# Optimization experiments

Hardware: AMD Instinct MI355X
Metric: run time of the kernel (lower is better)

The kernel has to match this reference:

```python
import jax, jax.numpy as jnp
import numpy as np

N, C, K, H = 100000, 128, 16, 128
MIX_IN = 2 * C + 1 + C   # x, mean_feat, boundary_score, coord_embed
GATE_IN = 2 * C + 1


def _mlp2(x, w1, b1, w2, b2):
    # Linear -> GELU(exact) -> Linear (dropout=0 at eval)
    return jax.nn.gelu(x @ w1 + b1, approximate=False) @ w2 + b2


def setup_inputs() -> dict:
    key = jax.random.key(0)
    ks = jax.random.split(key, 16)
    s = 0.02
    return {
        "feats": jax.random.normal(ks[0], (N, C), jnp.float32),
        "points": jax.random.normal(ks[1], (N, 3), jnp.float32),
        "neighbors": jax.random.randint(ks[2], (N, K), 0, N, jnp.int64),
        "ln_g": jnp.ones((C,), jnp.float32),
        "ln_b": jnp.zeros((C,), jnp.float32),
        "cp_w1": jax.random.normal(ks[3], (3, H), jnp.float32) * s,
        "cp_b1": jnp.zeros((H,), jnp.float32),
        "cp_w2": jax.random.normal(ks[4], (H, C), jnp.float32) * s,
        "cp_b2": jnp.zeros((C,), jnp.float32),
        "bd_w1": jax.random.normal(ks[5], (2, H), jnp.float32) * s,
        "bd_b1": jnp.zeros((H,), jnp.float32),
        "bd_w2": jax.random.normal(ks[6], (H, 1), jnp.float32) * s,
        "bd_b2": jnp.zeros((1,), jnp.float32),
        "mix_w1": jax.random.normal(ks[7], (MIX_IN, H), jnp.float32) * s,
        "mix_b1": jnp.zeros((H,), jnp.float32),
        "mix_w2": jax.random.normal(ks[8], (H, C), jnp.float32) * s,
        "mix_b2": jnp.zeros((C,), jnp.float32),
        "gate_w1": jax.random.normal(ks[9], (GATE_IN, H), jnp.float32) * s,
        "gate_b1": jnp.zeros((H,), jnp.float32),
        "gate_w2": jax.random.normal(ks[10], (H, C), jnp.float32) * s,
        "gate_b2": jnp.zeros((C,), jnp.float32),
        "out_w": jax.random.normal(ks[11], (C, C), jnp.float32) * s,
        "out_b": jnp.zeros((C,), jnp.float32),
    }


def _forward(feats, points, neighbors, ln_g, ln_b, cp_w1, cp_b1, cp_w2, cp_b2,
             bd_w1, bd_b1, bd_w2, bd_b2, mix_w1, mix_b1, mix_w2, mix_b2,
             gate_w1, gate_b1, gate_w2, gate_b2, out_w, out_b):
    n = feats.shape[0]
    # LayerNorm (eps=1e-5, torch default)
    mu = feats.mean(-1, keepdims=True)
    var = jnp.mean((feats - mu) ** 2, -1, keepdims=True)
    x = (feats - mu) * jax.lax.rsqrt(var + 1e-5) * ln_g + ln_b

    # sanitize neighbors
    valid = ((neighbors >= 0) & (neighbors < n)).astype(x.dtype)  # [N,K]
    safe = jnp.clip(neighbors, 0, n - 1)

    neigh_feats = x[safe]        # [N,K,C]
    neigh_points = points[safe]  # [N,K,3]
    denom = jnp.maximum(valid.sum(1, keepdims=True), 1.0)  # [N,1]
    w = valid[..., None]
    mean_feat = (neigh_feats * w).sum(1) / denom    # [N,C]
    mean_point = (neigh_points * w).sum(1) / denom  # [N,3]

    feat_diff = jnp.linalg.norm(x - mean_feat, axis=-1, keepdims=True)       # [N,1]
    coord_diff = jnp.linalg.norm(points - mean_point, axis=-1, keepdims=True)

    boundary = jax.nn.sigmoid(_mlp2(jnp.concatenate([feat_diff, coord_diff], -1),
                                    bd_w1, bd_b1, bd_w2, bd_b2))  # [N,1]

    # normalize points globally
    centered = points - points.mean(0, keepdims=True)
    scale = jnp.maximum(jnp.abs(centered).max(0, keepdims=True), 1e-6)
    coord_embed = _mlp2(centered / scale, cp_w1, cp_b1, cp_w2, cp_b2)  # [N,C]

    refined = _mlp2(jnp.concatenate([x, mean_feat, boundary, coord_embed], -1),
                    mix_w1, mix_b1, mix_w2, mix_b2)
    gate = jax.nn.sigmoid(_mlp2(jnp.concatenate([x, mean_feat, boundary], -1),
                                gate_w1, gate_b1, gate_w2, gate_b2))
    refined = (gate * refined) @ out_w + out_b
    return feats + refined


def reference(feats, points, neighbors, ln_g, ln_b, cp_w1, cp_b1, cp_w2, cp_b2,
              bd_w1, bd_b1, bd_w2, bd_b2, mix_w1, mix_b1, mix_w2, mix_b2,
              gate_w1, gate_b1, gate_w2, gate_b2, out_w, out_b):
    return _forward(feats, points, neighbors, ln_g, ln_b, cp_w1, cp_b1, cp_w2, cp_b2,
                    bd_w1, bd_b1, bd_w2, bd_b2, mix_w1, mix_b1, mix_w2, mix_b2,
                    gate_w1, gate_b1, gate_w2, gate_b2, out_w, out_b)
```

## Files before the change

kernel.cpp:

```cpp
#include <hip/hip_runtime.h>
#include <math.h>

constexpr int C    = 128;
constexpr int K    = 16;
constexpr int H    = 128;
constexpr int NB2  = 256;
constexpr int WPTS = 32;
constexpr int PB   = 128;
constexpr int HSU  = 68;

constexpr int WT_MIX   = 0;
constexpr int WT_GATE  = 49152;
constexpr int WT_CP2   = 81920;
constexpr int WT_MIX2  = 98304;
constexpr int WT_GATE2 = 114688;
constexpr int WT_OUT   = 131072;
constexpr int WT_TOTAL = 147456;

typedef __attribute__((ext_vector_type(8))) short short8;
typedef __attribute__((ext_vector_type(4))) float f32x4;
typedef _Float16 h2 __attribute__((ext_vector_type(2)));

__device__ __forceinline__ short f2bf(float f) {
    unsigned u = __float_as_uint(f);
    unsigned r = (u + 0x7fffu + ((u >> 16) & 1u)) >> 16;
    return (short)r;
}
__device__ __forceinline__ unsigned cvt_pk_bf16(float lo, float hi) {
    unsigned r;
    asm("v_cvt_pk_bf16_f32 %0, %1, %2" : "=v"(r) : "v"(lo), "v"(hi));
    return r;
}
__device__ __forceinline__ float bflo(unsigned v) { return __uint_as_float(v << 16); }
__device__ __forceinline__ float bfhi(unsigned v) { return __uint_as_float(v & 0xffff0000u); }
__device__ __forceinline__ float rcpf(float v) { return __builtin_amdgcn_rcpf(v); }

__device__ __forceinline__ unsigned f2e5m2(float x) {
    union { _Float16 h; unsigned short u; } cv;
    cv.h = (_Float16)x;
    return ((unsigned)cv.u + 0x7Fu + ((cv.u >> 8) & 1u)) >> 8;
}

__device__ __forceinline__ float gelu_f(float x) {
    float a = fabsf(x) * 0.70710678118654752440f;
    float t = rcpf(1.0f + 0.3275911f * a);
    float p = t * (0.254829592f + t * (-0.284496736f + t * (1.421413741f
            + t * (-1.453152027f + t * 1.061405429f))));
    float e = __expf(-a * a);
    float er = 1.0f - p * e;
    return 0.5f * x * (1.0f + copysignf(er, x));
}
__device__ __forceinline__ float sigm(float v) { return rcpf(1.0f + __expf(-v)); }

__global__ __launch_bounds__(256) void prep_all(
    const float* __restrict__ mix_w1, const float* __restrict__ gate_w1,
    const float* __restrict__ cp_w2,  const float* __restrict__ mix_w2,
    const float* __restrict__ gate_w2, const float* __restrict__ out_w,
    const float* __restrict__ points, const float* __restrict__ feats,
    const float* __restrict__ ln_g, const float* __restrict__ ln_b,
    short* __restrict__ wt, unsigned* __restrict__ xb,
    unsigned short* __restrict__ xg, float* __restrict__ pts4,
    float* __restrict__ partial, int n, int np4)
{
    __shared__ float sm[256];
    const int b   = blockIdx.x;
    const int tid = threadIdx.x;

    if (b < 36) {
        const float* src; int off; int c; bool skip256 = false;
        if (b < 12)      { src = mix_w1;  off = WT_MIX;   c = b;      skip256 = true; }
        else if (b < 20) { src = gate_w1; off = WT_GATE;  c = b - 12; }
        else if (b < 24) { src = cp_w2;   off = WT_CP2;   c = b - 20; }
        else if (b < 28) { src = mix_w2;  off = WT_MIX2;  c = b - 24; }
        else if (b < 32) { src = gate_w2; off = WT_GATE2; c = b - 28; }
        else             { src = out_w;   off = WT_OUT;   c = b - 32; }
        for (int ii = 0; ii < 16; ++ii) {
            int e = ii * 256 + tid;
            int j = e & 7, l = (e >> 3) & 63, t = e >> 9;
            int k = c * 32 + ((l >> 4) * 8) + j;
            int nn = t * 16 + (l & 15);
            int kk = (skip256 && k >= 256) ? k + 1 : k;
            wt[off + c * 4096 + e] = f2bf(src[kk * C + nn]);
        }
        return;
    }
    if (b == 36) {
        if (tid < 64) xb[(size_t)n * 64 + tid] = 0u;
        else if (tid < 96) ((unsigned*)xg)[(size_t)n * 32 + (tid - 64)] = 0u;
        return;
    }
    if (b < 37 + np4) {
        int i = (b - 37) * 256 + tid;
        if (i < n) {
            pts4[i * 4 + 0] = points[i * 3 + 0];
            pts4[i * 4 + 1] = points[i * 3 + 1];
            pts4[i * 4 + 2] = points[i * 3 + 2];
            pts4[i * 4 + 3] = 0.0f;
        } else if (i == n) {
            pts4[i * 4 + 0] = 0.0f; pts4[i * 4 + 1] = 0.0f;
            pts4[i * 4 + 2] = 0.0f; pts4[i * 4 + 3] = 0.0f;
        }
        return;
    }
    if (b < 37 + np4 + NB2) {
        const int bb = b - 37 - np4;
        float s[3] = {0, 0, 0};
        float mn[3] = {1e30f, 1e30f, 1e30f};
        float mx[3] = {-1e30f, -1e30f, -1e30f};
        for (int i = bb * 256 + tid; i < n; i += NB2 * 256) {
            #pragma unroll
            for (int c = 0; c < 3; ++c) {
                float v = points[i * 3 + c];
                s[c] += v; mn[c] = fminf(mn[c], v); mx[c] = fmaxf(mx[c], v);
            }
        }
        for (int q = 0; q < 9; ++q) {
            float v = (q < 3) ? s[q] : (q < 6) ? mn[q - 3] : mx[q - 6];
            sm[tid] = v;
            __syncthreads();
            for (int o = 128; o > 0; o >>= 1) {
                if (tid < o) {
                    float a = sm[tid], c = sm[tid + o];
                    sm[tid] = (q < 3) ? a + c : (q < 6) ? fminf(a, c) : fmaxf(a, c);
                }
                __syncthreads();
            }
            if (tid == 0) partial[bb * 9 + q] = sm[0];
            __syncthreads();
        }
        return;
    }

    const int lane = tid & 63;
    const int wave = tid >> 6;
    const int i = (b - 37 - np4 - NB2) * 4 + wave;
    if (i >= n) return;
    const float2 f = *(const float2*)(feats + i * C + 2 * lane);
    float s = f.x + f.y;
    #pragma unroll
    for (int o = 32; o > 0; o >>= 1) s += __shfl_xor(s, o, 64);
    const float mu = s * (1.0f / C);
    const float d0 = f.x - mu, d1 = f.y - mu;
    float v = d0 * d0 + d1 * d1;
    #pragma unroll
    for (int o = 32; o > 0; o >>= 1) v += __shfl_xor(v, o, 64);
    const float rs = rsqrtf(v * (1.0f / C) + 1e-5f);
    const float x0 = d0 * rs * ln_g[2 * lane] + ln_b[2 * lane];
    const float x1 = d1 * rs * ln_g[2 * lane + 1] + ln_b[2 * lane + 1];
    xb[(size_t)i * 64 + lane] =
        (unsigned)(unsigned short)f2bf(x0) | ((unsigned)(unsigned short)f2bf(x1) << 16);
    xg[(size_t)i * 64 + lane] =
        (unsigned short)(f2e5m2(x0) | (f2e5m2(x1) << 8));
}

__global__ __launch_bounds__(256, 2) void main_kernel(
    const unsigned* __restrict__ xb, const unsigned* __restrict__ xg,
    const float* __restrict__ pts4, const float* __restrict__ feats,
    const int* __restrict__ neighbors,
    const float* __restrict__ partial, const short* __restrict__ wt,
    const float* __restrict__ cp_w1, const float* __restrict__ cp_b1,
    const float* __restrict__ cp_b2,
    const float* __restrict__ bd_w1, const float* __restrict__ bd_b1,
    const float* __restrict__ bd_w2, const float* __restrict__ bd_b2,
    const float* __restrict__ mix_w1, const float* __restrict__ mix_b1,
    const float* __restrict__ mix_b2,
    const float* __restrict__ gate_w1, const float* __restrict__ gate_b1,
    const float* __restrict__ gate_b2,
    const float* __restrict__ out_b,
    float* __restrict__ out, int n)
{
    __shared__ __align__(16) char lds[71168];
    unsigned* mf_s  = (unsigned*)lds;
    unsigned* hid_s = (unsigned*)(lds + 34816);
    float* denom_s  = (float*)(lds + 69632);
    float* cd_s     = denom_s + 128;
    float* bd_s     = cd_s + 128;

    const int tid  = threadIdx.x;
    const int lane = tid & 63;
    const int w    = tid >> 6;
    const int m16  = lane & 15;
    const int h4   = lane >> 4;
    const int i0   = blockIdx.x * PB;
    const int wv32 = w * WPTS;
    const int i0w  = i0 + wv32;
    int* nb_w = (int*)(hid_s + (size_t)wv32 * HSU);

    {
        const int p0 = lane >> 2;
        const int jb = 4 * (lane & 3);
        const int r0 = min(i0w + p0, n - 1);
        const int r1 = min(i0w + 16 + p0, n - 1);
        const int4 A0 = *(const int4*)(neighbors + (size_t)r0 * K + jb);
        const int4 A1 = *(const int4*)(neighbors + (size_t)r1 * K + jb);

        const int q00 = ((unsigned)A0.x < (unsigned)n) ? A0.x : n;
        const int q01 = ((unsigned)A0.y < (unsigned)n) ? A0.y : n;
        const int q02 = ((unsigned)A0.z < (unsigned)n) ? A0.z : n;
        const int q03 = ((unsigned)A0.w < (unsigned)n) ? A0.w : n;
        const int q10 = ((unsigned)A1.x < (unsigned)n) ? A1.x : n;
        const int q11 = ((unsigned)A1.y < (unsigned)n) ? A1.y : n;
        const int q12 = ((unsigned)A1.z < (unsigned)n) ? A1.z : n;
        const int q13 = ((unsigned)A1.w < (unsigned)n) ? A1.w : n;

        *(int4*)&nb_w[4 * lane]       = make_int4(q00, q01, q02, q03);
        *(int4*)&nb_w[256 + 4 * lane] = make_int4(q10, q11, q12, q13);

        float c0 = (float)((q00 != n) + (q01 != n) + (q02 != n) + (q03 != n));
        float c1 = (float)((q10 != n) + (q11 != n) + (q12 != n) + (q13 != n));
        c0 += __shfl_xor(c0, 1, 64); c0 += __shfl_xor(c0, 2, 64);
        c1 += __shfl_xor(c1, 1, 64); c1 += __shfl_xor(c1, 2, 64);
        const float d0 = fmaxf(c0, 1.0f), d1 = fmaxf(c1, 1.0f);
        if ((lane & 3) == 0) {
            denom_s[wv32 + p0]      = d0;
            denom_s[wv32 + 16 + p0] = d1;
        }

        f32x4 s0 = *(const f32x4*)(pts4 + 4 * q00);
        s0 += *(const f32x4*)(pts4 + 4 * q01);
        s0 += *(const f32x4*)(pts4 + 4 * q02);
        s0 += *(const f32x4*)(pts4 + 4 * q03);
        f32x4 s1 = *(const f32x4*)(pts4 + 4 * q10);
        s1 += *(const f32x4*)(pts4 + 4 * q11);
        s1 += *(const f32x4*)(pts4 + 4 * q12);
        s1 += *(const f32x4*)(pts4 + 4 * q13);
        #pragma unroll
        for (int c = 0; c < 3; ++c) {
            s0[c] += __shfl_xor(s0[c], 1, 64); s0[c] += __shfl_xor(s0[c], 2, 64);
            s1[c] += __shfl_xor(s1[c], 1, 64); s1[c] += __shfl_xor(s1[c], 2, 64);
        }
        if ((lane & 3) == 0) {
            const float rd0 = rcpf(d0), rd1 = rcpf(d1);
            const f32x4 pv0 = *(const f32x4*)(pts4 + 4 * r0);
            const f32x4 pv1 = *(const f32x4*)(pts4 + 4 * r1);
            const float e00 = pv0[0] - s0[0] * rd0, e01 = pv0[1] - s0[1] * rd0, e02 = pv0[2] - s0[2] * rd0;
            const float e10 = pv1[0] - s1[0] * rd1, e11 = pv1[1] - s1[1] * rd1, e12 = pv1[2] - s1[2] * rd1;
            cd_s[wv32 + p0]      = sqrtf(e00 * e00 + e01 * e01 + e02 * e02);
            cd_s[wv32 + 16 + p0] = sqrtf(e10 * e10 + e11 * e11 + e12 * e12);
        }
    }

    float mean0, mean1, mean2, rsc0, rsc1, rsc2;
    {
        float sx = 0, sy = 0, sz = 0;
        float mnx = 1e30f, mny = 1e30f, mnz = 1e30f;
        float mxx = -1e30f, mxy = -1e30f, mxz = -1e30f;
        #pragma unroll
        for (int t = 0; t < 4; ++t) {
            const float* pp = partial + (size_t)(lane + 64 * t) * 9;
            sx += pp[0]; sy += pp[1]; sz += pp[2];
            mnx = fminf(mnx, pp[3]); mny = fminf(mny, pp[4]); mnz = fminf(mnz, pp[5]);
            mxx = fmaxf(mxx, pp[6]); mxy = fmaxf(mxy, pp[7]); mxz = fmaxf(mxz, pp[8]);
        }
        #pragma unroll
        for (int o = 32; o > 0; o >>= 1) {
            sx += __shfl_xor(sx, o, 64); sy += __shfl_xor(sy, o, 64); sz += __shfl_xor(sz, o, 64);
            mnx = fminf(mnx, __shfl_xor(mnx, o, 64));
            mny = fminf(mny, __shfl_xor(mny, o, 64));
            mnz = fminf(mnz, __shfl_xor(mnz, o, 64));
            mxx = fmaxf(mxx, __shfl_xor(mxx, o, 64));
            mxy = fmaxf(mxy, __shfl_xor(mxy, o, 64));
            mxz = fmaxf(mxz, __shfl_xor(mxz, o, 64));
        }
        const float fn = (float)n;
        mean0 = sx / fn; mean1 = sy / fn; mean2 = sz / fn;
        rsc0 = rcpf(fmaxf(fmaxf(mxx - mean0, mean0 - mnx), 1e-6f));
        rsc1 = rcpf(fmaxf(fmaxf(mxy - mean1, mean1 - mny), 1e-6f));
        rsc2 = rcpf(fmaxf(fmaxf(mxz - mean2, mean2 - mnz), 1e-6f));
    }

    {
        const int ul   = lane & 31;
        const int half = lane >> 5;
        float w1f[4], w1c[4], b1v[4], w2v[4];
        #pragma unroll
        for (int j = 0; j < 4; ++j) {
            int u = ul + 32 * j;
            w1f[j] = bd_w1[u]; w1c[j] = bd_w1[H + u];
            b1v[j] = bd_b1[u]; w2v[j] = bd_w2[u];
        }
        const float bb2 = bd_b2[0];

        unsigned B0[16], B1[16], B2[16], B3[16];

        auto bstep = [&](unsigned (&cur)[16], unsigned (&pf)[16], int pr, bool do_pf) {
            if (do_pf) {
                #pragma unroll
                for (int k = 0; k < K; ++k)
                    pf[k] = xg[(size_t)nb_w[((pr + 2) * 2 + half) * K + k] * 32 + ul];
            }
            union UH { unsigned u; h2 h; };
            UH a02, a13; a02.u = 0u; a13.u = 0u;
            #pragma unroll
            for (int k = 0; k < K; ++k) {
                const unsigned u = cur[k];
                UH lo, hi;
                lo.u = (u << 8) & 0xFF00FF00u;
                hi.u = u & 0xFF00FF00u;
                a02.h += lo.h;
                a13.h += hi.h;
            }
            float f0 = (float)a02.h[0], f2 = (float)a02.h[1];
            float f1 = (float)a13.h[0], f3 = (float)a13.h[1];

            const int p = 2 * pr + half;
            const float rden = rcpf(denom_s[wv32 + p]);
            f0 *= rden; f1 *= rden; f2 *= rden; f3 *= rden;
            uint2 pk;
            pk.x = cvt_pk_bf16(f0, f1);
            pk.y = cvt_pk_bf16(f2, f3);
            *(uint2*)(mf_s + (size_t)(wv32 + p) * HSU + 2 * ul) = pk;

            const int ipp = min(i0w + p, n - 1);
            const uint2 xv = *(const uint2*)(xb + (size_t)ipp * 64 + 2 * ul);
            const float d0 = bflo(xv.x) - f0, d1 = bfhi(xv.x) - f1;
            const float d2 = bflo(xv.y) - f2, d3 = bfhi(xv.y) - f3;
            float ss = d0 * d0 + d1 * d1 + d2 * d2 + d3 * d3;
            #pragma unroll
            for (int o = 16; o > 0; o >>= 1) ss += __shfl_xor(ss, o, 64);
            const float fd = sqrtf(ss);
            const float cd = cd_s[wv32 + p];
            float s = 0.0f;
            #pragma unroll
            for (int j = 0; j < 4; ++j)
                s += gelu_f(fd * w1f[j] + cd * w1c[j] + b1v[j]) * w2v[j];
            #pragma unroll
            for (int o = 16; o > 0; o >>= 1) s += __shfl_xor(s, o, 64);
            if (ul == 0) bd_s[wv32 + p] = sigm(s + bb2);
        };

        #pragma unroll
        for (int k = 0; k < K; ++k)
            B0[k] = xg[(size_t)nb_w[(0 + half) * K + k] * 32 + ul];
        #pragma unroll
        for (int k = 0; k < K; ++k)
            B1[k] = xg[(size_t)nb_w[(2 + half) * K + k] * 32 + ul];

        for (int g = 0; g < 3; ++g) {
            const int pr = 4 * g;
            bstep(B0, B2, pr + 0, true);
            bstep(B1, B3, pr + 1, true);
            bstep(B2, B0, pr + 2, true);
            bstep(B3, B1, pr + 3, true);
        }
        bstep(B0, B2, 12, true);
        bstep(B1, B3, 13, true);
        bstep(B2, B0, 14, false);
        bstep(B3, B1, 15, false);
    }

    const int pr0 = wv32 + m16, pr1 = wv32 + 16 + m16;
    const int ig0 = i0 + pr0,   ig1 = i0 + pr1;
    const int ip0 = min(ig0, n - 1), ip1 = min(ig1, n - 1);
    const unsigned* xr0  = xb + (size_t)ip0 * 64;
    const unsigned* xr1  = xb + (size_t)ip1 * 64;
    const unsigned* mfr0 = mf_s + pr0 * HSU;
    const unsigned* mfr1 = mf_s + pr1 * HSU;
    unsigned* hr0 = hid_s + pr0 * HSU;
    unsigned* hr1 = hid_s + pr1 * HSU;

    const float bdp0 = bd_s[pr0], bdp1 = bd_s[pr1];

    {
        f32x4 a0[8], a1[8];
        #pragma unroll
        for (int t = 0; t < 8; ++t) { a0[t] = (f32x4)0.0f; a1[t] = (f32x4)0.0f; }
        __builtin_amdgcn_s_setprio(1);
        #pragma unroll
        for (int c = 0; c < 8; ++c) {
            short8 af0, af1;
            if (c < 4) {
                af0 = *(const short8*)(xr0 + c * 16 + h4 * 4);
                af1 = *(const short8*)(xr1 + c * 16 + h4 * 4);
            } else {
                af0 = *(const short8*)(mfr0 + (c - 4) * 16 + h4 * 4);
                af1 = *(const short8*)(mfr1 + (c - 4) * 16 + h4 * 4);
            }
            const short* wgc = wt + WT_GATE + c * 4096 + lane * 8;
            #pragma unroll
            for (int t = 0; t < 8; ++t) {
                const short8 wf = *(const short8*)(wgc + t * 512);
                a0[t] = __builtin_amdgcn_mfma_f32_16x16x32_bf16(wf, af0, a0[t], 0, 0, 0);
                a1[t] = __builtin_amdgcn_mfma_f32_16x16x32_bf16(wf, af1, a1[t], 0, 0, 0);
            }
        }
        __builtin_amdgcn_s_setprio(0);
        #pragma unroll
        for (int t = 0; t < 8; ++t) {
            const int col = t * 16 + h4 * 4;
            const f32x4 wb = *(const f32x4*)(gate_w1 + 256 * C + col);
            const f32x4 bb = *(const f32x4*)(gate_b1 + col);
            const f32x4 v0 = a0[t] + bdp0 * wb + bb;
            const f32x4 v1 = a1[t] + bdp1 * wb + bb;
            uint2 pk0, pk1;
            pk0.x = cvt_pk_bf16(gelu_f(v0[0]), gelu_f(v0[1]));
            pk0.y = cvt_pk_bf16(gelu_f(v0[2]), gelu_f(v0[3]));
            pk1.x = cvt_pk_bf16(gelu_f(v1[0]), gelu_f(v1[1]));
            pk1.y = cvt_pk_bf16(gelu_f(v1[2]), gelu_f(v1[3]));
            *(uint2*)(hr0 + 8 * t + 2 * h4) = pk0;
            *(uint2*)(hr1 + 8 * t + 2 * h4) = pk1;
        }
    }

    uint2 gpk0[8], gpk1[8];
    {
        f32x4 a0[8], a1[8];
        #pragma unroll
        for (int t = 0; t < 8; ++t) { a0[t] = (f32x4)0.0f; a1[t] = (f32x4)0.0f; }
        __builtin_amdgcn_s_setprio(1);
        #pragma unroll
        for (int c = 0; c < 4; ++c) {
            const short8 af0 = *(const short8*)(hr0 + c * 16 + h4 * 4);
            const short8 af1 = *(const short8*)(hr1 + c * 16 + h4 * 4);
            const short* wgc = wt + WT_GATE2 + c * 4096 + lane * 8;
            #pragma unroll
            for (int t = 0; t < 8; ++t) {
                const short8 wf = *(const short8*)(wgc + t * 512);
                a0[t] = __builtin_amdgcn_mfma_f32_16x16x32_bf16(wf, af0, a0[t], 0, 0, 0);
                a1[t] = __builtin_amdgcn_mfma_f32_16x16x32_bf16(wf, af1, a1[t], 0, 0, 0);
            }
        }
        __builtin_amdgcn_s_setprio(0);
        #pragma unroll
        for (int t = 0; t < 8; ++t) {
            const f32x4 bb = *(const f32x4*)(gate_b2 + t * 16 + h4 * 4);
            gpk0[t].x = cvt_pk_bf16(sigm(a0[t][0] + bb[0]), sigm(a0[t][1] + bb[1]));
            gpk0[t].y = cvt_pk_bf16(sigm(a0[t][2] + bb[2]), sigm(a0[t][3] + bb[3]));
            gpk1[t].x = cvt_pk_bf16(sigm(a1[t][0] + bb[0]), sigm(a1[t][1] + bb[1]));
            gpk1[t].y = cvt_pk_bf16(sigm(a1[t][2] + bb[2]), sigm(a1[t][3] + bb[3]));
        }
    }

    {
        const f32x4 pv0 = *(const f32x4*)(pts4 + 4 * ip0);
        const f32x4 pv1 = *(const f32x4*)(pts4 + 4 * ip1);
        const float px0 = (pv0[0] - mean0) * rsc0;
        const float py0 = (pv0[1] - mean1) * rsc1;
        const float pz0 = (pv0[2] - mean2) * rsc2;
        const float px1 = (pv1[0] - mean0) * rsc0;
        const float py1 = (pv1[1] - mean1) * rsc1;
        const float pz1 = (pv1[2] - mean2) * rsc2;
        f32x4 a0[8], a1[8];
        #pragma unroll
        for (int t = 0; t < 8; ++t) { a0[t] = (f32x4)0.0f; a1[t] = (f32x4)0.0f; }
        #pragma unroll
        for (int c = 0; c < 4; ++c) {
            union { unsigned u[4]; short8 s; } cu0, cu1;
            #pragma unroll
            for (int jj = 0; jj < 4; ++jj) {
                const int hh = c * 32 + h4 * 8 + 2 * jj;
                const float wa0 = cp_w1[hh],     wb0 = cp_w1[H + hh],     wc0 = cp_w1[2 * H + hh];
                const float wa1 = cp_w1[hh + 1], wb1 = cp_w1[H + hh + 1], wc1 = cp_w1[2 * H + hh + 1];
                const float bb0 = cp_b1[hh], bb1 = cp_b1[hh + 1];
                cu0.u[jj] = cvt_pk_bf16(gelu_f(bb0 + px0 * wa0 + py0 * wb0 + pz0 * wc0),
                                        gelu_f(bb1 + px0 * wa1 + py0 * wb1 + pz0 * wc1));
                cu1.u[jj] = cvt_pk_bf16(gelu_f(bb0 + px1 * wa0 + py1 * wb0 + pz1 * wc0),
                                        gelu_f(bb1 + px1 * wa1 + py1 * wb1 + pz1 * wc1));
            }
            const short* wcp = wt + WT_CP2 + c * 4096 + lane * 8;
            __builtin_amdgcn_s_setprio(1);
            #pragma unroll
            for (int t = 0; t < 8; ++t) {
                const short8 wf = *(const short8*)(wcp + t * 512);
                a0[t] = __builtin_amdgcn_mfma_f32_16x16x32_bf16(wf, cu0.s, a0[t], 0, 0, 0);
                a1[t] = __builtin_amdgcn_mfma_f32_16x16x32_bf16(wf, cu1.s, a1[t], 0, 0, 0);
            }
            __builtin_amdgcn_s_setprio(0);
        }
        #pragma unroll
        for (int t = 0; t < 8; ++t) {
            const f32x4 bb = *(const f32x4*)(cp_b2 + t * 16 + h4 * 4);
            const f32x4 v0 = a0[t] + bb, v1 = a1[t] + bb;
            uint2 pk0, pk1;
            pk0.x = cvt_pk_bf16(v0[0], v0[1]); pk0.y = cvt_pk_bf16(v0[2], v0[3]);
            pk1.x = cvt_pk_bf16(v1[0], v1[1]); pk1.y = cvt_pk_bf16(v1[2], v1[3]);
            *(uint2*)(hr0 + 8 * t + 2 * h4) = pk0;
            *(uint2*)(hr1 + 8 * t + 2 * h4) = pk1;
        }
    }

    {
        f32x4 a0[8], a1[8];
        #pragma unroll
        for (int t = 0; t < 8; ++t) { a0[t] = (f32x4)0.0f; a1[t] = (f32x4)0.0f; }
        __builtin_amdgcn_s_setprio(1);
        #pragma unroll
        for (int c = 0; c < 12; ++c) {
            short8 af0, af1;
            if (c < 4) {
                af0 = *(const short8*)(xr0 + c * 16 + h4 * 4);
                af1 = *(const short8*)(xr1 + c * 16 + h4 * 4);
            } else if (c < 8) {
                af0 = *(const short8*)(mfr0 + (c - 4) * 16 + h4 * 4);
                af1 = *(const short8*)(mfr1 + (c - 4) * 16 + h4 * 4);
            } else {
                af0 = *(const short8*)(hr0 + (c - 8) * 16 + h4 * 4);
                af1 = *(const short8*)(hr1 + (c - 8) * 16 + h4 * 4);
            }
            const short* wmc = wt + WT_MIX + c * 4096 + lane * 8;
            #pragma unroll
            for (int t = 0; t < 8; ++t) {
                const short8 wf = *(const short8*)(wmc + t * 512);
                a0[t] = __builtin_amdgcn_mfma_f32_16x16x32_bf16(wf, af0, a0[t], 0, 0, 0);
                a1[t] = __builtin_amdgcn_mfma_f32_16x16x32_bf16(wf, af1, a1[t], 0, 0, 0);
            }
        }
        __builtin_amdgcn_s_setprio(0);
        #pragma unroll
        for (int t = 0; t < 8; ++t) {
            const int col = t * 16 + h4 * 4;
            const f32x4 wb = *(const f32x4*)(mix_w1 + 256 * C + col);
            const f32x4 bb = *(const f32x4*)(mix_b1 + col);
            const f32x4 v0 = a0[t] + bdp0 * wb + bb;
            const f32x4 v1 = a1[t] + bdp1 * wb + bb;
            uint2 pk0, pk1;
            pk0.x = cvt_pk_bf16(gelu_f(v0[0]), gelu_f(v0[1]));
            pk0.y = cvt_pk_bf16(gelu_f(v0[2]), gelu_f(v0[3]));
            pk1.x = cvt_pk_bf16(gelu_f(v1[0]), gelu_f(v1[1]));
            pk1.y = cvt_pk_bf16(gelu_f(v1[2]), gelu_f(v1[3]));
            *(uint2*)(hr0 + 8 * t + 2 * h4) = pk0;
            *(uint2*)(hr1 + 8 * t + 2 * h4) = pk1;
        }
    }

    {
        f32x4 a0[8], a1[8];
        #pragma unroll
        for (int t = 0; t < 8; ++t) { a0[t] = (f32x4)0.0f; a1[t] = (f32x4)0.0f; }
        __builtin_amdgcn_s_setprio(1);
        #pragma unroll
        for (int c = 0; c < 4; ++c) {
            const short8 af0 = *(const short8*)(hr0 + c * 16 + h4 * 4);
            const short8 af1 = *(const short8*)(hr1 + c * 16 + h4 * 4);
            const short* wmc = wt + WT_MIX2 + c * 4096 + lane * 8;
            #pragma unroll
            for (int t = 0; t < 8; ++t) {
                const short8 wf = *(const short8*)(wmc + t * 512);
                a0[t] = __builtin_amdgcn_mfma_f32_16x16x32_bf16(wf, af0, a0[t], 0, 0, 0);
                a1[t] = __builtin_amdgcn_mfma_f32_16x16x32_bf16(wf, af1, a1[t], 0, 0, 0);
            }
        }
        __builtin_amdgcn_s_setprio(0);
        #pragma unroll
        for (int t = 0; t < 8; ++t) {
            const f32x4 bb = *(const f32x4*)(mix_b2 + t * 16 + h4 * 4);
            const f32x4 v0 = a0[t] + bb, v1 = a1[t] + bb;
            uint2 pk0, pk1;
            pk0.x = cvt_pk_bf16(bflo(gpk0[t].x) * v0[0], bfhi(gpk0[t].x) * v0[1]);
            pk0.y = cvt_pk_bf16(bflo(gpk0[t].y) * v0[2], bfhi(gpk0[t].y) * v0[3]);
            pk1.x = cvt_pk_bf16(bflo(gpk1[t].x) * v1[0], bfhi(gpk1[t].x) * v1[1]);
            pk1.y = cvt_pk_bf16(bflo(gpk1[t].y) * v1[2], bfhi(gpk1[t].y) * v1[3]);
            *(uint2*)(hr0 + 8 * t + 2 * h4) = pk0;
            *(uint2*)(hr1 + 8 * t + 2 * h4) = pk1;
        }
    }

    {
        f32x4 a0[8], a1[8];
        #pragma unroll
        for (int t = 0; t < 8; ++t) { a0[t] = (f32x4)0.0f; a1[t] = (f32x4)0.0f; }
        __builtin_amdgcn_s_setprio(1);
        #pragma unroll
        for (int c = 0; c < 4; ++c) {
            const short8 af0 = *(const short8*)(hr0 + c * 16 + h4 * 4);
            const short8 af1 = *(const short8*)(hr1 + c * 16 + h4 * 4);
            const short* woc = wt + WT_OUT + c * 4096 + lane * 8;
            #pragma unroll
            for (int t = 0; t < 8; ++t) {
                const short8 wf = *(const short8*)(woc + t * 512);
                a0[t] = __builtin_amdgcn_mfma_f32_16x16x32_bf16(wf, af0, a0[t], 0, 0, 0);
                a1[t] = __builtin_amdgcn_mfma_f32_16x16x32_bf16(wf, af1, a1[t], 0, 0, 0);
            }
        }
        __builtin_amdgcn_s_setprio(0);
        #pragma unroll
        for (int t = 0; t < 8; ++t) {
            const int col = t * 16 + h4 * 4;
            const f32x4 bb = *(const f32x4*)(out_b + col);
            const f32x4 fv0 = *(const f32x4*)(feats + (size_t)ip0 * C + col);
            const f32x4 fv1 = *(const f32x4*)(feats + (size_t)ip1 * C + col);
            const f32x4 v0 = a0[t] + bb + fv0;
            const f32x4 v1 = a1[t] + bb + fv1;
            if (ig0 < n) *(f32x4*)(out + (size_t)ig0 * C + col) = v0;
            if (ig1 < n) *(f32x4*)(out + (size_t)ig1 * C + col) = v1;
        }
    }
}

extern "C" void kernel_launch(void* const* d_in, const int* in_sizes, int n_in,
                              void* d_out, int out_size, void* d_ws, size_t ws_size,
                              hipStream_t stream)
{
    const float* feats     = (const float*)d_in[0];
    const float* points    = (const float*)d_in[1];
    const int*   neighbors = (const int*)d_in[2];
    const float* ln_g      = (const float*)d_in[3];
    const float* ln_b      = (const float*)d_in[4];
    const float* cp_w1     = (const float*)d_in[5];
    const float* cp_b1     = (const float*)d_in[6];
    const float* cp_w2     = (const float*)d_in[7];
    const float* cp_b2     = (const float*)d_in[8];
    const float* bd_w1     = (const float*)d_in[9];
    const float* bd_b1     = (const float*)d_in[10];
    const float* bd_w2     = (const float*)d_in[11];
    const float* bd_b2     = (const float*)d_in[12];
    const float* mix_w1    = (const float*)d_in[13];
    const float* mix_b1    = (const float*)d_in[14];
    const float* mix_w2    = (const float*)d_in[15];
    const float* mix_b2    = (const float*)d_in[16];
    const float* gate_w1   = (const float*)d_in[17];
    const float* gate_b1   = (const float*)d_in[18];
    const float* gate_w2   = (const float*)d_in[19];
    const float* gate_b2   = (const float*)d_in[20];
    const float* out_w     = (const float*)d_in[21];
    const float* out_b     = (const float*)d_in[22];
    float* out = (float*)d_out;
    (void)n_in; (void)out_size; (void)ws_size;

    const int n = in_sizes[0] / C;

    char* base = (char*)d_ws;
    unsigned* xb        = (unsigned*)base;
    unsigned short* xg  = (unsigned short*)(base + (size_t)(n + 1) * 256);
    float* pts4         = (float*)(base + (size_t)(n + 1) * 384);
    short* wt           = (short*)((char*)pts4 + (size_t)(n + 1) * 16);
    float* partial      = (float*)((char*)wt + (size_t)WT_TOTAL * 2);

    const int np4 = (n + 256) / 256;
    const int nln = (n + 3) / 4;
    const int nb_main = (n + PB - 1) / PB;

    prep_all<<<37 + np4 + NB2 + nln, 256, 0, stream>>>(
        mix_w1, gate_w1, cp_w2, mix_w2, gate_w2, out_w,
        points, feats, ln_g, ln_b,
        wt, xb, xg, pts4, partial, n, np4);
    main_kernel<<<nb_main, 256, 0, stream>>>(
        xb, (const unsigned*)xg, pts4, feats, neighbors, partial, wt,
        cp_w1, cp_b1, cp_b2, bd_w1, bd_b1, bd_w2, bd_b2,
        mix_w1, mix_b1, mix_b2, gate_w1, gate_b1, gate_b2,
        out_b, out, n);
}
```

Measured before the change: 309.2 us.

## Process each wave's 32 points in two 16-point passes to double occupancy

Each wave now handles its 32 points as two sequential passes of 16 rows instead of running two 16-row MFMA tiles in parallel. This halves the accumulator registers and shrinks the LDS staging buffers (mf_s stride reduced, neighbor lists split into two buffers), so launch bounds can be raised from 2 to 4 blocks per CU. The intent is more waves in flight to hide the random neighbor gathers. The cost is that each weight fragment loaded from global memory now feeds one MFMA instead of two, doubling weight traffic per point.

```diff
diff --git a/kernel.cpp b/kernel.cpp
--- a/kernel.cpp
+++ b/kernel.cpp
@@ -8,6 +8,7 @@
 constexpr int WPTS = 32;
 constexpr int PB   = 128;
 constexpr int HSU  = 68;
+constexpr int MFU  = 66;
 
 constexpr int WT_MIX   = 0;
 constexpr int WT_GATE  = 49152;
@@ -153,7 +154,7 @@
         (unsigned short)(f2e5m2(x0) | (f2e5m2(x1) << 8));
 }
 
-__global__ __launch_bounds__(256, 2) void main_kernel(
+__global__ __launch_bounds__(256, 4) void main_kernel(
     const unsigned* __restrict__ xb, const unsigned* __restrict__ xg,
     const float* __restrict__ pts4, const float* __restrict__ feats,
     const int* __restrict__ neighbors,
@@ -169,12 +170,13 @@
     const float* __restrict__ out_b,
     float* __restrict__ out, int n)
 {
-    __shared__ __align__(16) char lds[71168];
+    __shared__ __align__(16) char lds[39936];
     unsigned* mf_s  = (unsigned*)lds;
-    unsigned* hid_s = (unsigned*)(lds + 34816);
-    float* denom_s  = (float*)(lds + 69632);
-    float* cd_s     = denom_s + 128;
-    float* bd_s     = cd_s + 128;
+    unsigned* hid_s = (unsigned*)(lds + 16896);
+    int*      nb1_s = (int*)(lds + 34304);
+    float* denom_s  = (float*)(lds + 38400);
+    float* cd_s     = (float*)(lds + 38912);
+    float* bd_s     = (float*)(lds + 39424);
 
     const int tid  = threadIdx.x;
     const int lane = tid & 63;
@@ -184,7 +186,8 @@
     const int i0   = blockIdx.x * PB;
     const int wv32 = w * WPTS;
     const int i0w  = i0 + wv32;
-    int* nb_w = (int*)(hid_s + (size_t)wv32 * HSU);
+    int* nb0_w = (int*)(hid_s + (size_t)w * 16 * HSU);
+    int* nb1_w = nb1_s + w * 256;
 
     {
         const int p0 = lane >> 2;
@@ -203,8 +206,8 @@
         const int q12 = ((unsigned)A1.z < (unsigned)n) ? A1.z : n;
         const int q13 = ((unsigned)A1.w < (unsigned)n) ? A1.w : n;
 
-        *(int4*)&nb_w[4 * lane]       = make_int4(q00, q01, q02, q03);
-        *(int4*)&nb_w[256 + 4 * lane] = make_int4(q10, q11, q12, q13);
+        *(int4*)&nb0_w[4 * lane] = make_int4(q00, q01, q02, q03);
+        *(int4*)&nb1_w[4 * lane] = make_int4(q10, q11, q12, q13);
 
         float c0 = (float)((q00 != n) + (q01 != n) + (q02 != n) + (q03 != n));
         float c1 = (float)((q10 != n) + (q11 != n) + (q12 != n) + (q13 != n));
@@ -269,320 +272,276 @@
         rsc2 = rcpf(fmaxf(fmaxf(mxz - mean2, mean2 - mnz), 1e-6f));
     }
 
-    {
-        const int ul   = lane & 31;
-        const int half = lane >> 5;
-        float w1f[4], w1c[4], b1v[4], w2v[4];
-        #pragma unroll
-        for (int j = 0; j < 4; ++j) {
-            int u = ul + 32 * j;
-            w1f[j] = bd_w1[u]; w1c[j] = bd_w1[H + u];
-            b1v[j] = bd_b1[u]; w2v[j] = bd_w2[u];
-        }
-        const float bb2 = bd_b2[0];
-
-        unsigned B0[16], B1[16], B2[16], B3[16];
-
-        auto bstep = [&](unsigned (&cur)[16], unsigned (&pf)[16], int pr, bool do_pf) {
-            if (do_pf) {
-                #pragma unroll
-                for (int k = 0; k < K; ++k)
-                    pf[k] = xg[(size_t)nb_w[((pr + 2) * 2 + half) * K + k] * 32 + ul];
-            }
-            union UH { unsigned u; h2 h; };
-            UH a02, a13; a02.u = 0u; a13.u = 0u;
-            #pragma unroll
-            for (int k = 0; k < K; ++k) {
-                const unsigned u = cur[k];
-                UH lo, hi;
-                lo.u = (u << 8) & 0xFF00FF00u;
-                hi.u = u & 0xFF00FF00u;
-                a02.h += lo.h;
-                a13.h += hi.h;
-            }
-            float f0 = (float)a02.h[0], f2 = (float)a02.h[1];
-            float f1 = (float)a13.h[0], f3 = (float)a13.h[1];
-
-            const int p = 2 * pr + half;
-            const float rden = rcpf(denom_s[wv32 + p]);
-            f0 *= rden; f1 *= rden; f2 *= rden; f3 *= rden;
-            uint2 pk;
-            pk.x = cvt_pk_bf16(f0, f1);
-            pk.y = cvt_pk_bf16(f2, f3);
-            *(uint2*)(mf_s + (size_t)(wv32 + p) * HSU + 2 * ul) = pk;
-
-            const int ipp = min(i0w + p, n - 1);
-            const uint2 xv = *(const uint2*)(xb + (size_t)ipp * 64 + 2 * ul);
-            const float d0 = bflo(xv.x) - f0, d1 = bfhi(xv.x) - f1;
-            const float d2 = bflo(xv.y) - f2, d3 = bfhi(xv.y) - f3;
-            float ss = d0 * d0 + d1 * d1 + d2 * d2 + d3 * d3;
-            #pragma unroll
-            for (int o = 16; o > 0; o >>= 1) ss += __shfl_xor(ss, o, 64);
-            const float fd = sqrtf(ss);
-            const float cd = cd_s[wv32 + p];
-            float s = 0.0f;
-            #pragma unroll
-            for (int j = 0; j < 4; ++j)
-                s += gelu_f(fd * w1f[j] + cd * w1c[j] + b1v[j]) * w2v[j];
-            #pragma unroll
-            for (int o = 16; o > 0; o >>= 1) s += __shfl_xor(s, o, 64);
-            if (ul == 0) bd_s[wv32 + p] = sigm(s + bb2);
-        };
-
-        #pragma unroll
-        for (int k = 0; k < K; ++k)
-            B0[k] = xg[(size_t)nb_w[(0 + half) * K + k] * 32 + ul];
-        #pragma unroll
-        for (int k = 0; k < K; ++k)
-            B1[k] = xg[(size_t)nb_w[(2 + half) * K + k] * 32 + ul];
-
-        for (int g = 0; g < 3; ++g) {
-            const int pr = 4 * g;
-            bstep(B0, B2, pr + 0, true);
-            bstep(B1, B3, pr + 1, true);
-            bstep(B2, B0, pr + 2, true);
-            bstep(B3, B1, pr + 3, true);
-        }
-        bstep(B0, B2, 12, true);
-        bstep(B1, B3, 13, true);
-        bstep(B2, B0, 14, false);
-        bstep(B3, B1, 15, false);
-    }
-
-    const int pr0 = wv32 + m16, pr1 = wv32 + 16 + m16;
-    const int ig0 = i0 + pr0,   ig1 = i0 + pr1;
-    const int ip0 = min(ig0, n - 1), ip1 = min(ig1, n - 1);
-    const unsigned* xr0  = xb + (size_t)ip0 * 64;
-    const unsigned* xr1  = xb + (size_t)ip1 * 64;
-    const unsigned* mfr0 = mf_s + pr0 * HSU;
-    const unsigned* mfr1 = mf_s + pr1 * HSU;
-    unsigned* hr0 = hid_s + pr0 * HSU;
-    unsigned* hr1 = hid_s + pr1 * HSU;
-
-    const float bdp0 = bd_s[pr0], bdp1 = bd_s[pr1];
-
-    {
-        f32x4 a0[8], a1[8];
-        #pragma unroll
-        for (int t = 0; t < 8; ++t) { a0[t] = (f32x4)0.0f; a1[t] = (f32x4)0.0f; }
-        __builtin_amdgcn_s_setprio(1);
-        #pragma unroll
-        for (int c = 0; c < 8; ++c) {
-            short8 af0, af1;
-            if (c < 4) {
-                af0 = *(const short8*)(xr0 + c * 16 + h4 * 4);
-                af1 = *(const short8*)(xr1 + c * 16 + h4 * 4);
-            } else {
-                af0 = *(const short8*)(mfr0 + (c - 4) * 16 + h4 * 4);
-                af1 = *(const short8*)(mfr1 + (c - 4) * 16 + h4 * 4);
-            }
-            const short* wgc = wt + WT_GATE + c * 4096 + lane * 8;
+    const int ul   = lane & 31;
+    const int half = lane >> 5;
+    float w1f[4], w1c[4], b1v[4], w2v[4];
+    #pragma unroll
+    for (int j = 0; j < 4; ++j) {
+        int u = ul + 32 * j;
+        w1f[j] = bd_w1[u]; w1c[j] = bd_w1[H + u];
+        b1v[j] = bd_b1[u]; w2v[j] = bd_w2[u];
+    }
+    const float bb2 = bd_b2[0];
+
+    #pragma unroll 1
+    for (int pass = 0; pass < 2; ++pass) {
+        const int pb    = pass * 16;
+        const int* nbp  = pass ? nb1_w : nb0_w;
+        const int ibase = i0w + pb;
+
+        {
+            unsigned B0[16], B1[16], B2[16], B3[16];
+
+            auto bstep = [&](unsigned (&cur)[16], unsigned (&pf)[16], int pr, bool do_pf) {
+                if (do_pf) {
+                    #pragma unroll
+                    for (int k = 0; k < K; ++k)
+                        pf[k] = xg[(size_t)nbp[((pr + 2) * 2 + half) * K + k] * 32 + ul];
+                }
+                union UH { unsigned u; h2 h; };
+                UH a02, a13; a02.u = 0u; a13.u = 0u;
+                #pragma unroll
+                for (int k = 0; k < K; ++k) {
+                    const unsigned u = cur[k];
+                    UH lo, hi;
+                    lo.u = (u << 8) & 0xFF00FF00u;
+                    hi.u = u & 0xFF00FF00u;
+                    a02.h += lo.h;
+                    a13.h += hi.h;
+                }
+                float f0 = (float)a02.h[0], f2 = (float)a02.h[1];
+                float f1 = (float)a13.h[0], f3 = (float)a13.h[1];
+
+                const int p = 2 * pr + half;
+                const float rden = rcpf(denom_s[wv32 + pb + p]);
+                f0 *= rden; f1 *= rden; f2 *= rden; f3 *= rden;
+                uint2 pk;
+                pk.x = cvt_pk_bf16(f0, f1);
+                pk.y = cvt_pk_bf16(f2, f3);
+                *(uint2*)(mf_s + (size_t)(w * 16 + p) * MFU + 2 * ul) = pk;
+
+                const int ipp = min(ibase + p, n - 1);
+                const uint2 xv = *(const uint2*)(xb + (size_t)ipp * 64 + 2 * ul);
+                const float d0 = bflo(xv.x) - f0, d1 = bfhi(xv.x) - f1;
+                const float d2 = bflo(xv.y) - f2, d3 = bfhi(xv.y) - f3;
+                float ss = d0 * d0 + d1 * d1 + d2 * d2 + d3 * d3;
+                #pragma unroll
+                for (int o = 16; o > 0; o >>= 1) ss += __shfl_xor(ss, o, 64);
+                const float fd = sqrtf(ss);
+                const float cd = cd_s[wv32 + pb + p];
+                float s = 0.0f;
+                #pragma unroll
+                for (int j = 0; j < 4; ++j)
+                    s += gelu_f(fd * w1f[j] + cd * w1c[j] + b1v[j]) * w2v[j];
+                #pragma unroll
+                for (int o = 16; o > 0; o >>= 1) s += __shfl_xor(s, o, 64);
+                if (ul == 0) bd_s[wv32 + pb + p] = sigm(s + bb2);
+            };
+
+            #pragma unroll
+            for (int k = 0; k < K; ++k)
+                B0[k] = xg[(size_t)nbp[(0 + half) * K + k] * 32 + ul];
+            #pragma unroll
+            for (int k = 0; k < K; ++k)
+                B1[k] = xg[(size_t)nbp[(2 + half) * K + k] * 32 + ul];
+
+            bstep(B0, B2, 0, true);
+            bstep(B1, B3, 1, true);
+            bstep(B2, B0, 2, true);
+            bstep(B3, B1, 3, true);
+            bstep(B0, B2, 4, true);
+            bstep(B1, B3, 5, true);
+            bstep(B2, B0, 6, false);
+            bstep(B3, B1, 7, false);
+        }
+
+        const int row = w * 16 + m16;
+        const int ig0 = i0 + wv32 + pb + m16;
+        const int ip0 = min(ig0, n - 1);
+        const unsigned* xr0  = xb + (size_t)ip0 * 64;
+        const unsigned* mfr0 = mf_s + row * MFU;
+        unsigned* hr0 = hid_s + row * HSU;
+        const float bdp0 = bd_s[wv32 + pb + m16];
+
+        {
+            f32x4 a[8];
+            #pragma unroll
+            for (int t = 0; t < 8; ++t) a[t] = (f32x4)0.0f;
+            __builtin_amdgcn_s_setprio(1);
+            #pragma unroll
+            for (int c = 0; c < 8; ++c) {
+                const short8 af = (c < 4)
+                    ? *(const short8*)(xr0 + c * 16 + h4 * 4)
+                    : *(const short8*)(mfr0 + (c - 4) * 16 + h4 * 4);
+                const short* wgc = wt + WT_GATE + c * 4096 + lane * 8;
+                #pragma unroll
+                for (int t = 0; t < 8; ++t) {
+                    const short8 wf = *(const short8*)(wgc + t * 512);
+                    a[t] = __builtin_amdgcn_mfma_f32_16x16x32_bf16(wf, af, a[t], 0, 0, 0);
+                }
+            }
+            __builtin_amdgcn_s_setprio(0);
             #pragma unroll
             for (int t = 0; t < 8; ++t) {
-                const short8 wf = *(const short8*)(wgc + t * 512);
-                a0[t] = __builtin_amdgcn_mfma_f32_16x16x32_bf16(wf, af0, a0[t], 0, 0, 0);
-                a1[t] = __builtin_amdgcn_mfma_f32_16x16x32_bf16(wf, af1, a1[t], 0, 0, 0);
-            }
-        }
-        __builtin_amdgcn_s_setprio(0);
-        #pragma unroll
-        for (int t = 0; t < 8; ++t) {
-            const int col = t * 16 + h4 * 4;
-            const f32x4 wb = *(const f32x4*)(gate_w1 + 256 * C + col);
-            const f32x4 bb = *(const f32x4*)(gate_b1 + col);
-            const f32x4 v0 = a0[t] + bdp0 * wb + bb;
-            const f32x4 v1 = a1[t] + bdp1 * wb + bb;
-            uint2 pk0, pk1;
-            pk0.x = cvt_pk_bf16(gelu_f(v0[0]), gelu_f(v0[1]));
-            pk0.y = cvt_pk_bf16(gelu_f(v0[2]), gelu_f(v0[3]));
-            pk1.x = cvt_pk_bf16(gelu_f(v1[0]), gelu_f(v1[1]));
-            pk1.y = cvt_pk_bf16(gelu_f(v1[2]), gelu_f(v1[3]));
-            *(uint2*)(hr0 + 8 * t + 2 * h4) = pk0;
-            *(uint2*)(hr1 + 8 * t + 2 * h4) = pk1;
-        }
-    }
-
-    uint2 gpk0[8], gpk1[8];
-    {
-        f32x4 a0[8], a1[8];
-        #pragma unroll
-        for (int t = 0; t < 8; ++t) { a0[t] = (f32x4)0.0f; a1[t] = (f32x4)0.0f; }
-        __builtin_amdgcn_s_setprio(1);
-        #pragma unroll
-        for (int c = 0; c < 4; ++c) {
-            const short8 af0 = *(const short8*)(hr0 + c * 16 + h4 * 4);
-            const short8 af1 = *(const short8*)(hr1 + c * 16 + h4 * 4);
-            const short* wgc = wt + WT_GATE2 + c * 4096 + lane * 8;
+                const int col = t * 16 + h4 * 4;
+                const f32x4 wb = *(const f32x4*)(gate_w1 + 256 * C + col);
+                const f32x4 bb = *(const f32x4*)(gate_b1 + col);
+                const f32x4 v = a[t] + bdp0 * wb + bb;
+                uint2 pk;
+                pk.x = cvt_pk_bf16(gelu_f(v[0]), gelu_f(v[1]));
+                pk.y = cvt_pk_bf16(gelu_f(v[2]), gelu_f(v[3]));
+                *(uint2*)(hr0 + 8 * t + 2 * h4) = pk;
+            }
+        }
+
+        uint2 gpk[8];
+        {
+            f32x4 a[8];
+            #pragma unroll
+            for (int t = 0; t < 8; ++t) a[t] = (f32x4)0.0f;
+            __builtin_amdgcn_s_setprio(1);
+            #pragma unroll
+            for (int c = 0; c < 4; ++c) {
+                const short8 af = *(const short8*)(hr0 + c * 16 + h4 * 4);
+                const short* wgc = wt + WT_GATE2 + c * 4096 + lane * 8;
+                #pragma unroll
+                for (int t = 0; t < 8; ++t) {
+                    const short8 wf = *(const short8*)(wgc + t * 512);
+                    a[t] = __builtin_amdgcn_mfma_f32_16x16x32_bf16(wf, af, a[t], 0, 0, 0);
+                }
+            }
+            __builtin_amdgcn_s_setprio(0);
             #pragma unroll
             for (int t = 0; t < 8; ++t) {
-                const short8 wf = *(const short8*)(wgc + t * 512);
-                a0[t] = __builtin_amdgcn_mfma_f32_16x16x32_bf16(wf, af0, a0[t], 0, 0, 0);
-                a1[t] = __builtin_amdgcn_mfma_f32_16x16x32_bf16(wf, af1, a1[t], 0, 0, 0);
-            }
-        }
-        __builtin_amdgcn_s_setprio(0);
-        #pragma unroll
-        for (int t = 0; t < 8; ++t) {
-            const f32x4 bb = *(const f32x4*)(gate_b2 + t * 16 + h4 * 4);
-            gpk0[t].x = cvt_pk_bf16(sigm(a0[t][0] + bb[0]), sigm(a0[t][1] + bb[1]));
-            gpk0[t].y = cvt_pk_bf16(sigm(a0[t][2] + bb[2]), sigm(a0[t][3] + bb[3]));
-            gpk1[t].x = cvt_pk_bf16(sigm(a1[t][0] + bb[0]), sigm(a1[t][1] + bb[1]));
-            gpk1[t].y = cvt_pk_bf16(sigm(a1[t][2] + bb[2]), sigm(a1[t][3] + bb[3]));
-        }
-    }
-
-    {
-        const f32x4 pv0 = *(const f32x4*)(pts4 + 4 * ip0);
-        const f32x4 pv1 = *(const f32x4*)(pts4 + 4 * ip1);
-        const float px0 = (pv0[0] - mean0) * rsc0;
-        const float py0 = (pv0[1] - mean1) * rsc1;
-        const float pz0 = (pv0[2] - mean2) * rsc2;
-        const float px1 = (pv1[0] - mean0) * rsc0;
-        const float py1 = (pv1[1] - mean1) * rsc1;
-        const float pz1 = (pv1[2] - mean2) * rsc2;
-        f32x4 a0[8], a1[8];
-        #pragma unroll
-        for (int t = 0; t < 8; ++t) { a0[t] = (f32x4)0.0f; a1[t] = (f32x4)0.0f; }
-        #pragma unroll
-        for (int c = 0; c < 4; ++c) {
-            union { unsigned u[4]; short8 s; } cu0, cu1;
-            #pragma unroll
-            for (int jj = 0; jj < 4; ++jj) {
-                const int hh = c * 32 + h4 * 8 + 2 * jj;
-                const float wa0 = cp_w1[hh],     wb0 = cp_w1[H + hh],     wc0 = cp_w1[2 * H + hh];
-                const float wa1 = cp_w1[hh + 1], wb1 = cp_w1[H + hh + 1], wc1 = cp_w1[2 * H + hh + 1];
-                const float bb0 = cp_b1[hh], bb1 = cp_b1[hh + 1];
-                cu0.u[jj] = cvt_pk_bf16(gelu_f(bb0 + px0 * wa0 + py0 * wb0 + pz0 * wc0),
-                                        gelu_f(bb1 + px0 * wa1 + py0 * wb1 + pz0 * wc1));
-                cu1.u[jj] = cvt_pk_bf16(gelu_f(bb0 + px1 * wa0 + py1 * wb0 + pz1 * wc0),
-                                        gelu_f(bb1 + px1 * wa1 + py1 * wb1 + pz1 * wc1));
-            }
-            const short* wcp = wt + WT_CP2 + c * 4096 + lane * 8;
+                const f32x4 bb = *(const f32x4*)(gate_b2 + t * 16 + h4 * 4);
+                gpk[t].x = cvt_pk_bf16(sigm(a[t][0] + bb[0]), sigm(a[t][1] + bb[1]));
+                gpk[t].y = cvt_pk_bf16(sigm(a[t][2] + bb[2]), sigm(a[t][3] + bb[3]));
+            }
+        }
+
+        {
+            const f32x4 pv = *(const f32x4*)(pts4 + 4 * ip0);
+            const float px = (pv[0] - mean0) * rsc0;
+            const float py = (pv[1] - mean1) * rsc1;
+            const float pz = (pv[2] - mean2) * rsc2;
+            f32x4 a[8];
+            #pragma unroll
+            for (int t = 0; t < 8; ++t) a[t] = (f32x4)0.0f;
+            #pragma unroll
+            for (int c = 0; c < 4; ++c) {
+                union { unsigned u[4]; short8 s; } cu;
+                #pragma unroll
+                for (int jj = 0; jj < 4; ++jj) {
+                    const int hh = c * 32 + h4 * 8 + 2 * jj;
+                    const float wa0 = cp_w1[hh],     wb0 = cp_w1[H + hh],     wc0 = cp_w1[2 * H + hh];
+                    const float wa1 = cp_w1[hh + 1], wb1 = cp_w1[H + hh + 1], wc1 = cp_w1[2 * H + hh + 1];
+                    const float bb0 = cp_b1[hh], bb1 = cp_b1[hh + 1];
+                    cu.u[jj] = cvt_pk_bf16(gelu_f(bb0 + px * wa0 + py * wb0 + pz * wc0),
+                                           gelu_f(bb1 + px * wa1 + py * wb1 + pz * wc1));
+                }
+                const short* wcp = wt + WT_CP2 + c * 4096 + lane * 8;
+                __builtin_amdgcn_s_setprio(1);
+                #pragma unroll
+                for (int t = 0; t < 8; ++t) {
+                    const short8 wf = *(const short8*)(wcp + t * 512);
+                    a[t] = __builtin_amdgcn_mfma_f32_16x16x32_bf16(wf, cu.s, a[t], 0, 0, 0);
+                }
+                __builtin_amdgcn_s_setprio(0);
+            }
+            #pragma unroll
+            for (int t = 0; t < 8; ++t) {
+                const f32x4 bb = *(const f32x4*)(cp_b2 + t * 16 + h4 * 4);
+                const f32x4 v = a[t] + bb;
+                uint2 pk;
+                pk.x = cvt_pk_bf16(v[0], v[1]);
+                pk.y = cvt_pk_bf16(v[2], v[3]);
+                *(uint2*)(hr0 + 8 * t + 2 * h4) = pk;
+            }
+        }
+
+        {
+            f32x4 a[8];
+            #pragma unroll
+            for (int t = 0; t < 8; ++t) a[t] = (f32x4)0.0f;
             __builtin_amdgcn_s_setprio(1);
             #pragma unroll
+            for (int c = 0; c < 12; ++c) {
+                short8 af;
+                if (c < 4)      af = *(const short8*)(xr0 + c * 16 + h4 * 4);
+                else if (c < 8) af = *(const short8*)(mfr0 + (c - 4) * 16 + h4 * 4);
+                else            af = *(const short8*)(hr0 + (c - 8) * 16 + h4 * 4);
+                const short* wmc = wt + WT_MIX + c * 4096 + lane * 8;
+                #pragma unroll
+                for (int t = 0; t < 8; ++t) {
+                    const short8 wf = *(const short8*)(wmc + t * 512);
+                    a[t] = __builtin_amdgcn_mfma_f32_16x16x32_bf16(wf, af, a[t], 0, 0, 0);
+                }
+            }
+            __builtin_amdgcn_s_setprio(0);
+            #pragma unroll
             for (int t = 0; t < 8; ++t) {
-                const short8 wf = *(const short8*)(wcp + t * 512);
-                a0[t] = __builtin_amdgcn_mfma_f32_16x16x32_bf16(wf, cu0.s, a0[t], 0, 0, 0);
-                a1[t] = __builtin_amdgcn_mfma_f32_16x16x32_bf16(wf, cu1.s, a1[t], 0, 0, 0);
+                const int col = t * 16 + h4 * 4;
+                const f32x4 wb = *(const f32x4*)(mix_w1 + 256 * C + col);
+                const f32x4 bb = *(const f32x4*)(mix_b1 + col);
+                const f32x4 v = a[t] + bdp0 * wb + bb;
+                uint2 pk;
+                pk.x = cvt_pk_bf16(gelu_f(v[0]), gelu_f(v[1]));
+                pk.y = cvt_pk_bf16(gelu_f(v[2]), gelu_f(v[3]));
+                *(uint2*)(hr0 + 8 * t + 2 * h4) = pk;
+            }
+        }
+
+        {
+            f32x4 a[8];
+            #pragma unroll
+            for (int t = 0; t < 8; ++t) a[t] = (f32x4)0.0f;
+            __builtin_amdgcn_s_setprio(1);
+            #pragma unroll
+            for (int c = 0; c < 4; ++c) {
+                const short8 af = *(const short8*)(hr0 + c * 16 + h4 * 4);
+                const short* wmc = wt + WT_MIX2 + c * 4096 + lane * 8;
+                #pragma unroll
+                for (int t = 0; t < 8; ++t) {
+                    const short8 wf = *(const short8*)(wmc + t * 512);
+                    a[t] = __builtin_amdgcn_mfma_f32_16x16x32_bf16(wf, af, a[t], 0, 0, 0);
+                }
             }
             __builtin_amdgcn_s_setprio(0);
-        }
-        #pragma unroll
-        for (int t = 0; t < 8; ++t) {
-            const f32x4 bb = *(const f32x4*)(cp_b2 + t * 16 + h4 * 4);
-            const f32x4 v0 = a0[t] + bb, v1 = a1[t] + bb;
-            uint2 pk0, pk1;
-            pk0.x = cvt_pk_bf16(v0[0], v0[1]); pk0.y = cvt_pk_bf16(v0[2], v0[3]);
-            pk1.x = cvt_pk_bf16(v1[0], v1[1]); pk1.y = cvt_pk_bf16(v1[2], v1[3]);
-            *(uint2*)(hr0 + 8 * t + 2 * h4) = pk0;
-            *(uint2*)(hr1 + 8 * t + 2 * h4) = pk1;
-        }
-    }
-
-    {
-        f32x4 a0[8], a1[8];
-        #pragma unroll
-        for (int t = 0; t < 8; ++t) { a0[t] = (f32x4)0.0f; a1[t] = (f32x4)0.0f; }
-        __builtin_amdgcn_s_setprio(1);
-        #pragma unroll
-        for (int c = 0; c < 12; ++c) {
-            short8 af0, af1;
-            if (c < 4) {
-                af0 = *(const short8*)(xr0 + c * 16 + h4 * 4);
-                af1 = *(const short8*)(xr1 + c * 16 + h4 * 4);
-            } else if (c < 8) {
-                af0 = *(const short8*)(mfr0 + (c - 4) * 16 + h4 * 4);
-                af1 = *(const short8*)(mfr1 + (c - 4) * 16 + h4 * 4);
-            } else {
-                af0 = *(const short8*)(hr0 + (c - 8) * 16 + h4 * 4);
-                af1 = *(const short8*)(hr1 + (c - 8) * 16 + h4 * 4);
-            }
-            const short* wmc = wt + WT_MIX + c * 4096 + lane * 8;
             #pragma unroll
             for (int t = 0; t < 8; ++t) {
-                const short8 wf = *(const short8*)(wmc + t * 512);
-                a0[t] = __builtin_amdgcn_mfma_f32_16x16x32_bf16(wf, af0, a0[t], 0, 0, 0);
-                a1[t] = __builtin_amdgcn_mfma_f32_16x16x32_bf16(wf, af1, a1[t], 0, 0, 0);
-            }
-        }
-        __builtin_amdgcn_s_setprio(0);
-        #pragma unroll
-        for (int t = 0; t < 8; ++t) {
-            const int col = t * 16 + h4 * 4;
-            const f32x4 wb = *(const f32x4*)(mix_w1 + 256 * C + col);
-            const f32x4 bb = *(const f32x4*)(mix_b1 + col);
-            const f32x4 v0 = a0[t] + bdp0 * wb + bb;
-            const f32x4 v1 = a1[t] + bdp1 * wb + bb;
-            uint2 pk0, pk1;
-            pk0.x = cvt_pk_bf16(gelu_f(v0[0]), gelu_f(v0[1]));
-            pk0.y = cvt_pk_bf16(gelu_f(v0[2]), gelu_f(v0[3]));
-            pk1.x = cvt_pk_bf16(gelu_f(v1[0]), gelu_f(v1[1]));
-            pk1.y = cvt_pk_bf16(gelu_f(v1[2]), gelu_f(v1[3]));
-            *(uint2*)(hr0 + 8 * t + 2 * h4) = pk0;
-            *(uint2*)(hr1 + 8 * t + 2 * h4) = pk1;
-        }
-    }
-
-    {
-        f32x4 a0[8], a1[8];
-        #pragma unroll
-        for (int t = 0; t < 8; ++t) { a0[t] = (f32x4)0.0f; a1[t] = (f32x4)0.0f; }
-        __builtin_amdgcn_s_setprio(1);
-        #pragma unroll
-        for (int c = 0; c < 4; ++c) {
-            const short8 af0 = *(const short8*)(hr0 + c * 16 + h4 * 4);
-            const short8 af1 = *(const short8*)(hr1 + c * 16 + h4 * 4);
-            const short* wmc = wt + WT_MIX2 + c * 4096 + lane * 8;
+                const f32x4 bb = *(const f32x4*)(mix_b2 + t * 16 + h4 * 4);
+                const f32x4 v = a[t] + bb;
+                uint2 pk;
+                pk.x = cvt_pk_bf16(bflo(gpk[t].x) * v[0], bfhi(gpk[t].x) * v[1]);
+                pk.y = cvt_pk_bf16(bflo(gpk[t].y) * v[2], bfhi(gpk[t].y) * v[3]);
+                *(uint2*)(hr0 + 8 * t + 2 * h4) = pk;
+            }
+        }
+
+        {
+            f32x4 a[8];
+            #pragma unroll
+            for (int t = 0; t < 8; ++t) a[t] = (f32x4)0.0f;
+            __builtin_amdgcn_s_setprio(1);
+            #pragma unroll
+            for (int c = 0; c < 4; ++c) {
+                const short8 af = *(const short8*)(hr0 + c * 16 + h4 * 4);
+                const short* woc = wt + WT_OUT + c * 4096 + lane * 8;
+                #pragma unroll
+                for (int t = 0; t < 8; ++t) {
+                    const short8 wf = *(const short8*)(woc + t * 512);
+                    a[t] = __builtin_amdgcn_mfma_f32_16x16x32_bf16(wf, af, a[t], 0, 0, 0);
+                }
+            }
+            __builtin_amdgcn_s_setprio(0);
             #pragma unroll
             for (int t = 0; t < 8; ++t) {
-                const short8 wf = *(const short8*)(wmc + t * 512);
-                a0[t] = __builtin_amdgcn_mfma_f32_16x16x32_bf16(wf, af0, a0[t], 0, 0, 0);
-                a1[t] = __builtin_amdgcn_mfma_f32_16x16x32_bf16(wf, af1, a1[t], 0, 0, 0);
-            }
-        }
-        __builtin_amdgcn_s_setprio(0);
-        #pragma unroll
-        for (int t = 0; t < 8; ++t) {
-            const f32x4 bb = *(const f32x4*)(mix_b2 + t * 16 + h4 * 4);
-            const f32x4 v0 = a0[t] + bb, v1 = a1[t] + bb;
-            uint2 pk0, pk1;
-            pk0.x = cvt_pk_bf16(bflo(gpk0[t].x) * v0[0], bfhi(gpk0[t].x) * v0[1]);
-            pk0.y = cvt_pk_bf16(bflo(gpk0[t].y) * v0[2], bfhi(gpk0[t].y) * v0[3]);
-            pk1.x = cvt_pk_bf16(bflo(gpk1[t].x) * v1[0], bfhi(gpk1[t].x) * v1[1]);
-            pk1.y = cvt_pk_bf16(bflo(gpk1[t].y) * v1[2], bfhi(gpk1[t].y) * v1[3]);
-            *(uint2*)(hr0 + 8 * t + 2 * h4) = pk0;
-            *(uint2*)(hr1 + 8 * t + 2 * h4) = pk1;
-        }
-    }
-
-    {
-        f32x4 a0[8], a1[8];
-        #pragma unroll
-        for (int t = 0; t < 8; ++t) { a0[t] = (f32x4)0.0f; a1[t] = (f32x4)0.0f; }
-        __builtin_amdgcn_s_setprio(1);
-        #pragma unroll
-        for (int c = 0; c < 4; ++c) {
-            const short8 af0 = *(const short8*)(hr0 + c * 16 + h4 * 4);
-            const short8 af1 = *(const short8*)(hr1 + c * 16 + h4 * 4);
-            const short* woc = wt + WT_OUT + c * 4096 + lane * 8;
-            #pragma unroll
-            for (int t = 0; t < 8; ++t) {
-                const short8 wf = *(const short8*)(woc + t * 512);
-                a0[t] = __builtin_amdgcn_mfma_f32_16x16x32_bf16(wf, af0, a0[t], 0, 0, 0);
-                a1[t] = __builtin_amdgcn_mfma_f32_16x16x32_bf16(wf, af1, a1[t], 0, 0, 0);
-            }
-        }
-        __builtin_amdgcn_s_setprio(0);
-        #pragma unroll
-        for (int t = 0; t < 8; ++t) {
-            const int col = t * 16 + h4 * 4;
-            const f32x4 bb = *(const f32x4*)(out_b + col);
-            const f32x4 fv0 = *(const f32x4*)(feats + (size_t)ip0 * C + col);
-            const f32x4 fv1 = *(const f32x4*)(feats + (size_t)ip1 * C + col);
-            const f32x4 v0 = a0[t] + bb + fv0;
-            const f32x4 v1 = a1[t] + bb + fv1;
-            if (ig0 < n) *(f32x4*)(out + (size_t)ig0 * C + col) = v0;
-            if (ig1 < n) *(f32x4*)(out + (size_t)ig1 * C + col) = v1;
+                const int col = t * 16 + h4 * 4;
+                const f32x4 bb = *(const f32x4*)(out_b + col);
+                const f32x4 fv = *(const f32x4*)(feats + (size_t)ip0 * C + col);
+                const f32x4 v = a[t] + bb + fv;
+                if (ig0 < n) *(f32x4*)(out + (size_t)ig0 * C + col) = v;
+            }
         }
     }
 }
```

Result: slower. 885.9 us (+186.6%).
